# Performance work log

Hardware: AMD Instinct MI355X
Metric: run time of the kernel (lower is better)

Reference implementation:

```python
import jax, jax.numpy as jnp
import numpy as np

HEADS = 8
DIM_HEAD = 64
QUERY_DIM = 1024
CONTEXT_DIM = 768
INNER = HEADS * DIM_HEAD  # 512


def setup_inputs() -> dict:
    key = jax.random.key(0)
    ks = jax.random.split(key, 7)
    B, Sq, Skv = 4, 4096, 1024
    x = jax.random.normal(ks[0], (B, Sq, QUERY_DIM), dtype=jnp.float32)
    context = jax.random.normal(ks[1], (B, Skv, CONTEXT_DIM), dtype=jnp.float32)
    # nn.Linear(in, out) weights stored as [out, in]; we use [in, out] for x @ W
    Wq = jax.random.normal(ks[2], (QUERY_DIM, INNER), dtype=jnp.float32) * (QUERY_DIM ** -0.5)
    Wk = jax.random.normal(ks[3], (CONTEXT_DIM, INNER), dtype=jnp.float32) * (CONTEXT_DIM ** -0.5)
    Wv = jax.random.normal(ks[4], (CONTEXT_DIM, INNER), dtype=jnp.float32) * (CONTEXT_DIM ** -0.5)
    Wo = jax.random.normal(ks[5], (INNER, QUERY_DIM), dtype=jnp.float32) * (INNER ** -0.5)
    bo = jax.random.normal(ks[6], (QUERY_DIM,), dtype=jnp.float32) * 0.01
    return {"x": x, "context": context, "Wq": Wq, "Wk": Wk, "Wv": Wv, "Wo": Wo, "bo": bo}


def reference(x, context, Wq, Wk, Wv, Wo, bo):
    B, Sq, _ = x.shape
    h, d = HEADS, DIM_HEAD
    scale = d ** -0.5
    # project and split heads: [B, S, h*d] -> [B, h, S, d]
    q = (x @ Wq).reshape(B, Sq, h, d).transpose(0, 2, 1, 3)
    k = (context @ Wk).reshape(B, -1, h, d).transpose(0, 2, 1, 3)
    v = (context @ Wv).reshape(B, -1, h, d).transpose(0, 2, 1, 3)
    # the torch chunked loop is exactly full softmax attention (softmax is row-wise)
    scores = jnp.einsum('bhid,bhjd->bhij', q, k) * scale
    attn = jax.nn.softmax(scores, axis=-1)
    out = jnp.einsum('bhij,bhjd->bhid', attn, v)  # [B, h, Sq, d]
    out = out.transpose(0, 2, 1, 3).reshape(B, Sq, h * d)
    return out @ Wo + bo
```

## Files before the change

### kernel.cpp

```cpp
#include <hip/hip_runtime.h>

#define SQ 4096
#define SKV 1024
#define BATCH 4
#define NH 8
#define DH 64
#define QD 1024
#define CD 768
#define INNER 512

typedef _Float16 half8 __attribute__((ext_vector_type(8)));
typedef _Float16 half4v __attribute__((ext_vector_type(4)));
typedef float floatx4 __attribute__((ext_vector_type(4)));
typedef float f32x16 __attribute__((ext_vector_type(16)));
typedef unsigned int uint4v __attribute__((ext_vector_type(4)));

#define MFMA16(a, b, c) __builtin_amdgcn_mfma_f32_16x16x32_f16(a, b, c, 0, 0, 0)
#define MFMA32(a, b, c) __builtin_amdgcn_mfma_f32_32x32x16_f16(a, b, c, 0, 0, 0)

#define PLSWAP(a, b) asm("v_permlane32_swap_b32 %0, %1" : "+v"(a), "+v"(b))

#define GLD16(gptr, lptr)                                                            \
  __builtin_amdgcn_global_load_lds(                                                  \
      (const __attribute__((address_space(1))) unsigned int*)(const void*)(gptr),    \
      (__attribute__((address_space(3))) unsigned int*)(void*)(lptr), 16, 0, 0)

__global__ __launch_bounds__(256) void cast_f2h(const float* __restrict__ x,
                                                const float* __restrict__ ctx,
                                                _Float16* __restrict__ xh,
                                                _Float16* __restrict__ ctxh) {
  const size_t NX = (size_t)BATCH * SQ * QD;
  size_t i = ((size_t)blockIdx.x * 256 + threadIdx.x) * 8;
  const float* s;
  _Float16* d;
  size_t off;
  if (i < NX) { s = x; d = xh; off = i; }
  else        { s = ctx; d = ctxh; off = i - NX; }
  floatx4 a = *(const floatx4*)(s + off);
  floatx4 b = *(const floatx4*)(s + off + 4);
  half8 h;
#pragma unroll
  for (int j = 0; j < 4; ++j) { h[j] = (_Float16)a[j]; h[4 + j] = (_Float16)b[j]; }
  *(half8*)(d + off) = h;
}

__global__ __launch_bounds__(256) void transpose_all(const float* __restrict__ Wq,
                                                     const float* __restrict__ Wk,
                                                     const float* __restrict__ Wv,
                                                     const float* __restrict__ Wo,
                                                     _Float16* __restrict__ wqt,
                                                     _Float16* __restrict__ wkvt,
                                                     _Float16* __restrict__ wot) {
  __shared__ float tile[32][33];
  const int z = blockIdx.z;
  const float* src; _Float16* dst; int R, C;
  if (z == 0)      { src = Wq; dst = wqt;                        R = QD;    C = INNER; }
  else if (z == 1) { src = Wk; dst = wkvt;                       R = CD;    C = INNER; }
  else if (z == 2) { src = Wv; dst = wkvt + (size_t)INNER * CD;  R = CD;    C = INNER; }
  else             { src = Wo; dst = wot;                        R = INNER; C = QD;   }
  const int c0 = blockIdx.x * 32, r0 = blockIdx.y * 32;
  if (c0 >= C || r0 >= R) return;
  const int tx = threadIdx.x & 31, ty = threadIdx.x >> 5;
#pragma unroll
  for (int i = 0; i < 32; i += 8)
    tile[ty + i][tx] = src[(size_t)(r0 + ty + i) * C + c0 + tx];
  __syncthreads();
#pragma unroll
  for (int i = 0; i < 32; i += 8)
    dst[(size_t)(c0 + ty + i) * R + r0 + tx] = (_Float16)tile[tx][ty + i];
}

template <int MODE>
__device__ __forceinline__ void gemm_body(const _Float16* __restrict__ A,
                                          const _Float16* __restrict__ Bt,
                                          void* __restrict__ Cout,
                                          void* __restrict__ Cout2,
                                          const float* __restrict__ bias,
                                          int M, int N, int K, int bx, int by,
                                          _Float16* As16, _Float16* Bs) {
  const int tid = threadIdx.x;
  const int wave = tid >> 6, lane = tid & 63;
  const int quad = lane >> 4, l16 = lane & 15;
  const int wm = (wave >> 1) * 64, wn = (wave & 1) * 64;
  const size_t n0 = (size_t)bx * 128, m0 = (size_t)by * 128;

  floatx4 acc[4][4] = {};

  const _Float16* ag = A + (m0 + (tid >> 2)) * (size_t)K + (tid & 3) * 8;
  const _Float16* bg = Bt + (n0 + (tid >> 2)) * (size_t)K + (tid & 3) * 8;

  for (int k0 = 0; k0 < K; k0 += 32) {
    __syncthreads();
#pragma unroll
    for (int j = 0; j < 2; ++j)
      GLD16(ag + k0 + (size_t)j * 64 * K, As16 + tid * 8 + j * 2048);
#pragma unroll
    for (int j = 0; j < 2; ++j)
      GLD16(bg + k0 + (size_t)j * 64 * K, Bs + tid * 8 + j * 2048);
    __syncthreads();

    half8 af[4], bf[4];
#pragma unroll
    for (int mt = 0; mt < 4; ++mt)
      af[mt] = *(const half8*)(As16 + (wm + mt * 16 + l16) * 32 + quad * 8);
#pragma unroll
    for (int nt = 0; nt < 4; ++nt)
      bf[nt] = *(const half8*)(Bs + (wn + nt * 16 + l16) * 32 + quad * 8);
#pragma unroll
    for (int mt = 0; mt < 4; ++mt)
#pragma unroll
      for (int nt = 0; nt < 4; ++nt)
        acc[mt][nt] = MFMA16(af[mt], bf[nt], acc[mt][nt]);
  }

  if (MODE == 3) {
    _Float16* C = (_Float16*)Cout;
    const float sc = 0.125f * 1.44269504088896f;
#pragma unroll
    for (int mt = 0; mt < 4; ++mt) {
      const size_t row = m0 + wm + mt * 16 + quad * 4;
#pragma unroll
      for (int nt = 0; nt < 4; ++nt) {
        const size_t col = n0 + wn + nt * 16 + l16;
#pragma unroll
        for (int r = 0; r < 4; ++r)
          C[(row + r) * N + col] = (_Float16)(acc[mt][nt][r] * sc);
      }
    }
  } else if (MODE == 4) {
    if (n0 < INNER) {
      _Float16* C = (_Float16*)Cout;
#pragma unroll
      for (int mt = 0; mt < 4; ++mt) {
        const size_t row = m0 + wm + mt * 16 + quad * 4;
#pragma unroll
        for (int nt = 0; nt < 4; ++nt) {
          const size_t col = n0 + wn + nt * 16 + l16;
#pragma unroll
          for (int r = 0; r < 4; ++r)
            C[(row + r) * INNER + col] = (_Float16)acc[mt][nt][r];
        }
      }
    } else {
      _Float16* C = (_Float16*)Cout2;
      const int b = (int)(m0 >> 10);
#pragma unroll
      for (int mt = 0; mt < 4; ++mt) {
        const int kvb = (int)(m0 & 1023) + wm + mt * 16 + quad * 4;
#pragma unroll
        for (int nt = 0; nt < 4; ++nt) {
          const int col = (int)(n0 - INNER + wn + nt * 16 + l16);
          const int h = col >> 6, d = col & 63;
          half4v pk;
#pragma unroll
          for (int r = 0; r < 4; ++r) pk[r] = (_Float16)acc[mt][nt][r];
          *(half4v*)(C + (size_t)((b * NH + h) * DH + d) * SKV + kvb) = pk;
        }
      }
    }
  } else {
    float* C = (float*)Cout;
#pragma unroll
    for (int mt = 0; mt < 4; ++mt) {
      const size_t row = m0 + wm + mt * 16 + quad * 4;
#pragma unroll
      for (int nt = 0; nt < 4; ++nt) {
        const size_t col = n0 + wn + nt * 16 + l16;
        const float bb = bias[col];
#pragma unroll
        for (int r = 0; r < 4; ++r)
          C[(row + r) * N + col] = acc[mt][nt][r] + bb;
      }
    }
  }
}

__global__ __launch_bounds__(256) void proj_fused(const _Float16* __restrict__ xh,
                                                  const _Float16* __restrict__ ctxh,
                                                  const _Float16* __restrict__ wqt,
                                                  const _Float16* __restrict__ wkvt,
                                                  _Float16* __restrict__ qh,
                                                  _Float16* __restrict__ kh,
                                                  _Float16* __restrict__ vth) {
  __shared__ _Float16 As16[128 * 32];
  __shared__ _Float16 Bs[128 * 32];
  const int id = blockIdx.x;
  const int seg = id % 3, base = id / 3;
  if (seg == 2) {
    gemm_body<4>(ctxh, wkvt, kh, vth, nullptr, BATCH * SKV, 2 * INNER, CD,
                 base & 7, base >> 3, As16, Bs);
  } else {
    const int q = base * 2 + seg;
    gemm_body<3>(xh, wqt, qh, nullptr, nullptr, BATCH * SQ, INNER, QD,
                 q & 3, q >> 2, As16, Bs);
  }
}

__global__ __launch_bounds__(256) void gemm_out(const _Float16* __restrict__ A,
                                                const _Float16* __restrict__ Bt,
                                                float* __restrict__ Cout,
                                                const float* __restrict__ bias) {
  __shared__ _Float16 As16[128 * 32];
  __shared__ _Float16 Bs[128 * 32];
  gemm_body<2>(A, Bt, Cout, nullptr, bias, BATCH * SQ, QD, INNER,
               blockIdx.x, blockIdx.y, As16, Bs);
}

__global__ __launch_bounds__(256, 3) void flash_attn7(const _Float16* __restrict__ Q,
                                                      const _Float16* __restrict__ Kp,
                                                      const _Float16* __restrict__ Vt,
                                                      _Float16* __restrict__ O) {
  __shared__ _Float16 Ksb[2 * 64 * 64];
  __shared__ _Float16 Vsb[2 * 64 * 64];
  const int tid = threadIdx.x;
  const int wave = tid >> 6, lane = tid & 63;
  const int l31 = lane & 31, hi = lane >> 5, x7 = lane & 7;

  const int flat = blockIdx.x;
  const int nf = (flat & 7) * 128 + (flat >> 3);
  const int qblk = nf & 31, bh = nf >> 5;
  const int b = bh >> 3, h = bh & 7;

  const size_t qrow0 = (size_t)b * SQ + qblk * 128 + wave * 32;
  const _Float16* qptr = Q + qrow0 * INNER + h * DH;
  const _Float16* kbase = Kp + (size_t)b * SKV * INNER + h * DH;
  const _Float16* vbase = Vt + (size_t)bh * DH * SKV;

  const int kr = tid >> 3;
  const int kb = (tid & 7) ^ (kr & 7);
  const _Float16* kg = kbase + (size_t)kr * INNER + kb * 8;
  const _Float16* vg = vbase + (size_t)kr * SKV + kb * 8;

#define STAGE_KV(bi, tt)                                                        \
  do {                                                                          \
    _Float16* _kl = Ksb + (bi) * 4096 + tid * 8;                                \
    _Float16* _vl = Vsb + (bi) * 4096 + tid * 8;                                \
    GLD16(kg + (size_t)((tt) * 64) * INNER, _kl);                               \
    GLD16(kg + (size_t)((tt) * 64 + 32) * INNER, _kl + 2048);                   \
    GLD16(vg + (tt) * 64, _vl);                                                 \
    GLD16(vg + (size_t)32 * SKV + (tt) * 64, _vl + 2048);                       \
  } while (0)

  half8 aq[4];
#pragma unroll
  for (int i = 0; i < 4; ++i)
    aq[i] = *(const half8*)(qptr + (size_t)l31 * INNER + i * 16 + hi * 8);

  int koff[4], voffB[4];
#pragma unroll
  for (int i = 0; i < 4; ++i)
    koff[i] = l31 * 64 + (((i * 2 + hi) ^ x7) << 3);
#pragma unroll
  for (int j = 0; j < 4; ++j)
    voffB[j] = l31 * 64 + (((j * 2 + hi) ^ x7) << 3);

  half8 ones;
#pragma unroll
  for (int j = 0; j < 8; ++j) ones[j] = (_Float16)1.0f;

  f32x16 o0 = {}, o1 = {}, osum = {};

  STAGE_KV(0, 0);

  for (int t = 0; t < SKV / 64; ++t) {
    __syncthreads();
    if (t < SKV / 64 - 1) STAGE_KV((t + 1) & 1, t + 1);
    const _Float16* ks = Ksb + (t & 1) * 4096;
    const _Float16* vs = Vsb + (t & 1) * 4096;

#pragma unroll
    for (int c2 = 0; c2 < 2; ++c2) {
      half8 ak[4];
#pragma unroll
      for (int i = 0; i < 4; ++i)
        ak[i] = *(const half8*)(ks + c2 * 2048 + koff[i]);

      f32x16 st = {};
#pragma unroll
      for (int i = 0; i < 4; ++i) st = MFMA32(ak[i], aq[i], st);

      unsigned w[8];
#pragma unroll
      for (int j = 0; j < 8; ++j) {
        float plo = __builtin_exp2f(st[2 * j]);
        float phi = __builtin_exp2f(st[2 * j + 1]);
        w[j] = __builtin_bit_cast(unsigned, __builtin_amdgcn_cvt_pkrtz(plo, phi));
      }
      PLSWAP(w[0], w[2]);
      PLSWAP(w[1], w[3]);
      PLSWAP(w[4], w[6]);
      PLSWAP(w[5], w[7]);
      uint4v u0 = {w[0], w[1], w[2], w[3]};
      uint4v u1 = {w[4], w[5], w[6], w[7]};
      half8 A0 = __builtin_bit_cast(half8, u0);
      half8 A1 = __builtin_bit_cast(half8, u1);

      osum = MFMA32(A0, ones, osum);
      osum = MFMA32(A1, ones, osum);

      {
        half8 bv00 = *(const half8*)(vs + 0 * 2048 + voffB[c2 * 2 + 0]);
        half8 bv10 = *(const half8*)(vs + 1 * 2048 + voffB[c2 * 2 + 0]);
        o0 = MFMA32(A0, bv00, o0);
        o1 = MFMA32(A0, bv10, o1);
        half8 bv01 = *(const half8*)(vs + 0 * 2048 + voffB[c2 * 2 + 1]);
        half8 bv11 = *(const half8*)(vs + 1 * 2048 + voffB[c2 * 2 + 1]);
        o0 = MFMA32(A1, bv01, o0);
        o1 = MFMA32(A1, bv11, o1);
      }
    }
  }

  float inv16[16];
#pragma unroll
  for (int r = 0; r < 16; ++r) inv16[r] = 1.0f / osum[r];

  _Float16* op = O + qrow0 * INNER + h * DH;
#pragma unroll
  for (int r = 0; r < 16; ++r) {
    const int q = (r & 3) + 8 * (r >> 2) + 4 * hi;
    op[(size_t)q * INNER + l31] = (_Float16)(o0[r] * inv16[r]);
    op[(size_t)q * INNER + 32 + l31] = (_Float16)(o1[r] * inv16[r]);
  }
#undef STAGE_KV
}

extern "C" void kernel_launch(void* const* d_in, const int* in_sizes, int n_in,
                              void* d_out, int out_size, void* d_ws, size_t ws_size,
                              hipStream_t stream) {
  const float* x   = (const float*)d_in[0];
  const float* ctx = (const float*)d_in[1];
  const float* Wq  = (const float*)d_in[2];
  const float* Wk  = (const float*)d_in[3];
  const float* Wv  = (const float*)d_in[4];
  const float* Wo  = (const float*)d_in[5];
  const float* bo  = (const float*)d_in[6];
  float* out = (float*)d_out;

  const size_t NX = (size_t)BATCH * SQ * QD;
  const size_t NC = (size_t)BATCH * SKV * CD;

  _Float16* ws = (_Float16*)d_ws;
  _Float16* xh   = ws;
  _Float16* ctxh = xh + NX;
  _Float16* wqt  = ctxh + NC;
  _Float16* wkvt = wqt + (size_t)INNER * QD;
  _Float16* wot  = wkvt + (size_t)2 * INNER * CD;
  _Float16* qh   = wot + (size_t)QD * INNER;
  _Float16* kh   = qh + (size_t)BATCH * SQ * INNER;
  _Float16* vth  = kh + (size_t)BATCH * SKV * INNER;
  _Float16* aoh  = xh;

  cast_f2h<<<dim3((unsigned)((NX + NC) / 2048)), 256, 0, stream>>>(x, ctx, xh, ctxh);

  transpose_all<<<dim3(32, 32, 4), 256, 0, stream>>>(Wq, Wk, Wv, Wo, wqt, wkvt, wot);

  proj_fused<<<dim3(768), 256, 0, stream>>>(xh, ctxh, wqt, wkvt, qh, kh, vth);

  flash_attn7<<<dim3(BATCH * NH * SQ / 128), 256, 0, stream>>>(qh, kh, vth, aoh);

  gemm_out<<<dim3(QD / 128, BATCH * SQ / 128), 256, 0, stream>>>(aoh, wot, out, bo);
}
```

Measured before the change: 270.6 us.

## Double-buffer GEMM LDS staging, merge prep kernels, add MFMA priority hints

Merges the fp16 cast kernel and the weight-transpose kernel into one prep launch, removing one launch and its gap. Double-buffers the shared-memory tiles in the projection and output GEMMs so the next K-slice loads while MFMAs run on the current one, leaving one barrier per iteration instead of two. Adds s_setprio around the MFMA blocks in both the GEMM and the attention kernel to favour issuing matrix instructions. The extra LDS buffers double shared-memory use per block, which may lower occupancy.

```diff
diff --git a/kernel.cpp b/kernel.cpp
--- a/kernel.cpp
+++ b/kernel.cpp
@@ -25,40 +25,45 @@
       (const __attribute__((address_space(1))) unsigned int*)(const void*)(gptr),    \
       (__attribute__((address_space(3))) unsigned int*)(void*)(lptr), 16, 0, 0)
 
-__global__ __launch_bounds__(256) void cast_f2h(const float* __restrict__ x,
-                                                const float* __restrict__ ctx,
-                                                _Float16* __restrict__ xh,
-                                                _Float16* __restrict__ ctxh) {
+__global__ __launch_bounds__(256) void prep(const float* __restrict__ x,
+                                            const float* __restrict__ ctx,
+                                            const float* __restrict__ Wq,
+                                            const float* __restrict__ Wk,
+                                            const float* __restrict__ Wv,
+                                            const float* __restrict__ Wo,
+                                            _Float16* __restrict__ xh,
+                                            _Float16* __restrict__ ctxh,
+                                            _Float16* __restrict__ wqt,
+                                            _Float16* __restrict__ wkvt,
+                                            _Float16* __restrict__ wot) {
+  __shared__ float tile[32][33];
   const size_t NX = (size_t)BATCH * SQ * QD;
-  size_t i = ((size_t)blockIdx.x * 256 + threadIdx.x) * 8;
-  const float* s;
-  _Float16* d;
-  size_t off;
-  if (i < NX) { s = x; d = xh; off = i; }
-  else        { s = ctx; d = ctxh; off = i - NX; }
-  floatx4 a = *(const floatx4*)(s + off);
-  floatx4 b = *(const floatx4*)(s + off + 4);
-  half8 h;
-#pragma unroll
-  for (int j = 0; j < 4; ++j) { h[j] = (_Float16)a[j]; h[4 + j] = (_Float16)b[j]; }
-  *(half8*)(d + off) = h;
-}
-
-__global__ __launch_bounds__(256) void transpose_all(const float* __restrict__ Wq,
-                                                     const float* __restrict__ Wk,
-                                                     const float* __restrict__ Wv,
-                                                     const float* __restrict__ Wo,
-                                                     _Float16* __restrict__ wqt,
-                                                     _Float16* __restrict__ wkvt,
-                                                     _Float16* __restrict__ wot) {
-  __shared__ float tile[32][33];
-  const int z = blockIdx.z;
+  const size_t NC = (size_t)BATCH * SKV * CD;
+  const unsigned NCAST = (unsigned)((NX + NC) / 2048);
+
+  if (blockIdx.x < NCAST) {
+    size_t i = ((size_t)blockIdx.x * 256 + threadIdx.x) * 8;
+    const float* s;
+    _Float16* d;
+    size_t off;
+    if (i < NX) { s = x; d = xh; off = i; }
+    else        { s = ctx; d = ctxh; off = i - NX; }
+    floatx4 a = *(const floatx4*)(s + off);
+    floatx4 b = *(const floatx4*)(s + off + 4);
+    half8 h;
+#pragma unroll
+    for (int j = 0; j < 4; ++j) { h[j] = (_Float16)a[j]; h[4 + j] = (_Float16)b[j]; }
+    *(half8*)(d + off) = h;
+    return;
+  }
+  const unsigned t = blockIdx.x - NCAST;
+  const int z = t >> 10, rem = t & 1023;
   const float* src; _Float16* dst; int R, C;
   if (z == 0)      { src = Wq; dst = wqt;                        R = QD;    C = INNER; }
   else if (z == 1) { src = Wk; dst = wkvt;                       R = CD;    C = INNER; }
   else if (z == 2) { src = Wv; dst = wkvt + (size_t)INNER * CD;  R = CD;    C = INNER; }
   else             { src = Wo; dst = wot;                        R = INNER; C = QD;   }
-  const int c0 = blockIdx.x * 32, r0 = blockIdx.y * 32;
+  const int c0 = (rem & 31) * 32, r0 = (rem >> 5) * 32;
   if (c0 >= C || r0 >= R) return;
   const int tx = threadIdx.x & 31, ty = threadIdx.x >> 5;
 #pragma unroll
@@ -89,29 +94,38 @@
   const _Float16* ag = A + (m0 + (tid >> 2)) * (size_t)K + (tid & 3) * 8;
   const _Float16* bg = Bt + (n0 + (tid >> 2)) * (size_t)K + (tid & 3) * 8;
 
-  for (int k0 = 0; k0 < K; k0 += 32) {
+#define GSTAGE(bi, k0)                                                      \
+  do {                                                                      \
+    GLD16(ag + (k0), As16 + (bi)*4096 + tid * 8);                           \
+    GLD16(ag + (k0) + (size_t)64 * K, As16 + (bi)*4096 + tid * 8 + 2048);   \
+    GLD16(bg + (k0), Bs + (bi)*4096 + tid * 8);                             \
+    GLD16(bg + (k0) + (size_t)64 * K, Bs + (bi)*4096 + tid * 8 + 2048);     \
+  } while (0)
+
+  const int NT = K / 32;
+  GSTAGE(0, 0);
+  for (int t = 0; t < NT; ++t) {
     __syncthreads();
-#pragma unroll
-    for (int j = 0; j < 2; ++j)
-      GLD16(ag + k0 + (size_t)j * 64 * K, As16 + tid * 8 + j * 2048);
-#pragma unroll
-    for (int j = 0; j < 2; ++j)
-      GLD16(bg + k0 + (size_t)j * 64 * K, Bs + tid * 8 + j * 2048);
-    __syncthreads();
+    if (t + 1 < NT) GSTAGE((t + 1) & 1, (t + 1) * 32);
+    const _Float16* as = As16 + (t & 1) * 4096;
+    const _Float16* bs = Bs + (t & 1) * 4096;
 
     half8 af[4], bf[4];
 #pragma unroll
     for (int mt = 0; mt < 4; ++mt)
-      af[mt] = *(const half8*)(As16 + (wm + mt * 16 + l16) * 32 + quad * 8);
+      af[mt] = *(const half8*)(as + (wm + mt * 16 + l16) * 32 + quad * 8);
 #pragma unroll
     for (int nt = 0; nt < 4; ++nt)
-      bf[nt] = *(const half8*)(Bs + (wn + nt * 16 + l16) * 32 + quad * 8);
+      bf[nt] = *(const half8*)(bs + (wn + nt * 16 + l16) * 32 + quad * 8);
+    __builtin_amdgcn_s_setprio(1);
 #pragma unroll
     for (int mt = 0; mt < 4; ++mt)
 #pragma unroll
       for (int nt = 0; nt < 4; ++nt)
         acc[mt][nt] = MFMA16(af[mt], bf[nt], acc[mt][nt]);
-  }
+    __builtin_amdgcn_s_setprio(0);
+  }
+#undef GSTAGE
 
   if (MODE == 3) {
     _Float16* C = (_Float16*)Cout;
@@ -182,8 +196,8 @@
                                                   _Float16* __restrict__ qh,
                                                   _Float16* __restrict__ kh,
                                                   _Float16* __restrict__ vth) {
-  __shared__ _Float16 As16[128 * 32];
-  __shared__ _Float16 Bs[128 * 32];
+  __shared__ _Float16 As16[2 * 128 * 32];
+  __shared__ _Float16 Bs[2 * 128 * 32];
   const int id = blockIdx.x;
   const int seg = id % 3, base = id / 3;
   if (seg == 2) {
@@ -200,8 +214,8 @@
                                                 const _Float16* __restrict__ Bt,
                                                 float* __restrict__ Cout,
                                                 const float* __restrict__ bias) {
-  __shared__ _Float16 As16[128 * 32];
-  __shared__ _Float16 Bs[128 * 32];
+  __shared__ _Float16 As16[2 * 128 * 32];
+  __shared__ _Float16 Bs[2 * 128 * 32];
   gemm_body<2>(A, Bt, Cout, nullptr, bias, BATCH * SQ, QD, INNER,
                blockIdx.x, blockIdx.y, As16, Bs);
 }
@@ -276,8 +290,10 @@
         ak[i] = *(const half8*)(ks + c2 * 2048 + koff[i]);
 
       f32x16 st = {};
+      __builtin_amdgcn_s_setprio(1);
 #pragma unroll
       for (int i = 0; i < 4; ++i) st = MFMA32(ak[i], aq[i], st);
+      __builtin_amdgcn_s_setprio(0);
 
       unsigned w[8];
 #pragma unroll
@@ -295,6 +311,7 @@
       half8 A0 = __builtin_bit_cast(half8, u0);
       half8 A1 = __builtin_bit_cast(half8, u1);
 
+      __builtin_amdgcn_s_setprio(1);
       osum = MFMA32(A0, ones, osum);
       osum = MFMA32(A1, ones, osum);
 
@@ -308,6 +325,7 @@
         o0 = MFMA32(A1, bv01, o0);
         o1 = MFMA32(A1, bv11, o1);
       }
+      __builtin_amdgcn_s_setprio(0);
     }
   }
 
@@ -351,9 +369,8 @@
   _Float16* vth  = kh + (size_t)BATCH * SKV * INNER;
   _Float16* aoh  = xh;
 
-  cast_f2h<<<dim3((unsigned)((NX + NC) / 2048)), 256, 0, stream>>>(x, ctx, xh, ctxh);
-
-  transpose_all<<<dim3(32, 32, 4), 256, 0, stream>>>(Wq, Wk, Wv, Wo, wqt, wkvt, wot);
+  prep<<<dim3((unsigned)((NX + NC) / 2048) + 4096), 256, 0, stream>>>(
+      x, ctx, Wq, Wk, Wv, Wo, xh, ctxh, wqt, wkvt, wot);
 
   proj_fused<<<dim3(768), 256, 0, stream>>>(xh, ctxh, wqt, wkvt, qh, kh, vth);
 
```

Measured after the change: 275.8 us. About the same (+2.0%).
